# Kernel tuning notes

Measured on AMD Instinct MI355X. Metric: run time of the kernel, lower is better.

Reference implementation:

```python
import jax, jax.numpy as jnp
import numpy as np

ALPHA = 0.2  # LeakyReLU negative slope
NEG_INF = -9e15


def setup_inputs() -> dict:
    key = jax.random.key(0)
    k1, k2, k3, k4, k5 = jax.random.split(key, 5)
    B, N, F_in, F_out = 1, 8192, 256, 128
    h = jax.random.normal(k1, (B, N, F_in), dtype=jnp.float32)
    adj_mat = jax.random.randint(k2, (B, N, N), 0, 2, dtype=jnp.int32)
    W = jax.random.normal(k3, (F_out, F_in), dtype=jnp.float32) * 0.05
    b = jax.random.normal(k4, (F_out,), dtype=jnp.float32) * 0.05
    a = jax.random.normal(k5, (2 * F_out, 1), dtype=jnp.float32) * 0.05
    return {"h": h, "adj_mat": adj_mat, "W": W, "b": b, "a": a}


def reference(h, adj_mat, W, b, a):
    # Wh: (B, N, F_out)
    Wh = jnp.einsum('bnf,of->bno', h, W) + b
    F_out = W.shape[0]
    # Original builds concat[Wh_i, Wh_j] @ a. Equivalent: a1.Wh_i + a2.Wh_j.
    a1 = a[:F_out, 0]
    a2 = a[F_out:, 0]
    s1 = Wh @ a1  # (B, N) source-i contribution
    s2 = Wh @ a2  # (B, N) source-j contribution
    e = s1[:, :, None] + s2[:, None, :]  # (B, N, N)
    e = jnp.where(e >= 0, e, ALPHA * e)  # LeakyReLU
    e = jnp.where(adj_mat > 0, e, NEG_INF)
    attention = jax.nn.softmax(e, axis=1)  # softmax over dim=1, as in the source
    h_prime = jnp.einsum('bij,bjf->bif', attention, Wh)
    return jax.nn.elu(h_prime)
```

## Files before the change

### kernel.cpp

```cpp
#include <hip/hip_runtime.h>

#define NN 8192
#define FI 256
#define FO 128
#define GAT_ALPHA 0.2f

typedef _Float16 f16x8 __attribute__((ext_vector_type(8)));
typedef _Float16 f16x2 __attribute__((ext_vector_type(2)));
typedef float f32x4 __attribute__((ext_vector_type(4)));
typedef unsigned char uchar;
typedef unsigned int uint32;

__global__ __launch_bounds__(256) void k1_wh(const float* __restrict__ h,
                                             const float* __restrict__ W,
                                             const float* __restrict__ bias,
                                             float* __restrict__ Wh) {
  __shared__ float hs[32][FI + 1];
  __shared__ float wt[32][FO];
  const int t = threadIdx.x;
  const int j0 = blockIdx.x * 32;
  {
    const int row = t >> 3, c0 = (t & 7) * 32;
    const float* src = h + (size_t)(j0 + row) * FI + c0;
#pragma unroll
    for (int e = 0; e < 8; ++e) {
      float4 v = *(const float4*)(src + 4 * e);
      hs[row][c0 + 4 * e + 0] = v.x;
      hs[row][c0 + 4 * e + 1] = v.y;
      hs[row][c0 + 4 * e + 2] = v.z;
      hs[row][c0 + 4 * e + 3] = v.w;
    }
  }
  const int f4 = (t & 31) * 4;
  const int r0 = (t >> 5) * 4;
  float acc[4][4];
#pragma unroll
  for (int r = 0; r < 4; ++r)
#pragma unroll
    for (int e = 0; e < 4; ++e) acc[r][e] = 0.f;

  for (int kc = 0; kc < FI; kc += 32) {
    __syncthreads();
    {
      const int f = t >> 1, kb = (t & 1) * 16;
      const float* wsrc = W + (size_t)f * FI + kc + kb;
#pragma unroll
      for (int e = 0; e < 16; ++e) wt[kb + e][f] = wsrc[e];
    }
    __syncthreads();
#pragma unroll
    for (int k = 0; k < 32; ++k) {
      const float4 wv = *(const float4*)&wt[k][f4];
      float hv[4];
#pragma unroll
      for (int r = 0; r < 4; ++r) hv[r] = hs[r0 + r][kc + k];
#pragma unroll
      for (int r = 0; r < 4; ++r) {
        acc[r][0] += hv[r] * wv.x;
        acc[r][1] += hv[r] * wv.y;
        acc[r][2] += hv[r] * wv.z;
        acc[r][3] += hv[r] * wv.w;
      }
    }
  }
  const float4 bv = *(const float4*)&bias[f4];
#pragma unroll
  for (int r = 0; r < 4; ++r) {
    float4 o;
    o.x = acc[r][0] + bv.x;
    o.y = acc[r][1] + bv.y;
    o.z = acc[r][2] + bv.z;
    o.w = acc[r][3] + bv.w;
    *(float4*)&Wh[(size_t)(j0 + r0 + r) * FO + f4] = o;
  }
}

__global__ __launch_bounds__(256) void k1b_sv(const float* __restrict__ Wh,
                                              const float* __restrict__ a,
                                              float4* __restrict__ r4,
                                              float4* __restrict__ c4,
                                              float2* __restrict__ r2,
                                              uint32* __restrict__ c2h,
                                              float* __restrict__ s2x,
                                              float* __restrict__ corr) {
  if (blockIdx.x == 0 && threadIdx.x < FO) corr[threadIdx.x] = 0.f;
  const int lane = threadIdx.x & 63;
  const int j = blockIdx.x * 4 + (threadIdx.x >> 6);
  const float* row = Wh + (size_t)j * FO;
  const float w0 = row[lane], w1 = row[lane + 64];
  float s1 = w0 * a[lane] + w1 * a[lane + 64];
  float s2 = w0 * a[FO + lane] + w1 * a[FO + lane + 64];
#pragma unroll
  for (int o = 32; o >= 1; o >>= 1) {
    s1 += __shfl_xor(s1, o);
    s2 += __shfl_xor(s2, o);
  }
  if (lane == 0) {
    const float e1 = expf(s1), e1a = expf(GAT_ALPHA * s1);
    const float e2 = expf(s2), e2a = expf(GAT_ALPHA * s2);
    float4 rv; rv.x = s1; rv.y = e1; rv.z = e1a; rv.w = 0.f;
    float4 cv; cv.x = s2; cv.y = e2; cv.z = e2a; cv.w = 0.f;
    r4[j] = rv;
    c4[j] = cv;
    r2[j] = make_float2(e1, e1a);
    f16x2 cp; cp.x = (_Float16)e2; cp.y = (_Float16)e2a;
    c2h[j] = __builtin_bit_cast(uint32, cp);
    s2x[j] = s2;
  }
}

__global__ __launch_bounds__(256) void k2_stats(const int* __restrict__ adj,
                                                const float4* __restrict__ r4,
                                                const float* __restrict__ s2x,
                                                uchar* __restrict__ bitsB,
                                                float2* __restrict__ zpart) {
  __shared__ float4 rs[64];
  const int t = threadIdx.x;
  const int jc = blockIdx.x & 3;
  const int ic = blockIdx.x >> 2;
  const int i0 = ic * 64;
  const int j0 = jc * 2048 + t * 8;
  if (t < 64) rs[t] = r4[i0 + t];
  const float4 ca = *(const float4*)(s2x + j0);
  const float4 cb = *(const float4*)(s2x + j0 + 4);
  const float cx[8] = {ca.x, ca.y, ca.z, ca.w, cb.x, cb.y, cb.z, cb.w};
  float accP[8], accN[8];
#pragma unroll
  for (int e = 0; e < 8; ++e) { accP[e] = 0.f; accN[e] = 0.f; }
  __syncthreads();
  const int4* ap = (const int4*)(adj + (size_t)i0 * NN + j0);
  uchar* bp = bitsB + (size_t)i0 * (NN / 8) + jc * 256 + t;
  for (int ir = 0; ir < 64; ir += 8) {
    int4 av[8][2];
#pragma unroll
    for (int u = 0; u < 8; ++u) {
      av[u][0] = ap[(size_t)(ir + u) * (NN / 4)];
      av[u][1] = ap[(size_t)(ir + u) * (NN / 4) + 1];
    }
#pragma unroll
    for (int u = 0; u < 8; ++u) {
      const float4 ri = rs[ir + u];
      const int aa[8] = {av[u][0].x, av[u][0].y, av[u][0].z, av[u][0].w,
                         av[u][1].x, av[u][1].y, av[u][1].z, av[u][1].w};
      uint32 byte = 0;
#pragma unroll
      for (int e = 0; e < 8; ++e) {
        const bool act = aa[e] > 0;
        byte |= act ? (1u << e) : 0u;
        const bool pos = (ri.x + cx[e]) >= 0.f;
        accP[e] += (act && pos) ? ri.y : 0.f;
        accN[e] += (act && !pos) ? ri.z : 0.f;
      }
      bp[(size_t)(ir + u) * (NN / 8)] = (uchar)byte;
    }
  }
  float2* zp = zpart + (size_t)ic * NN + j0;
#pragma unroll
  for (int e = 0; e < 8; ++e) zp[e] = make_float2(accP[e], accN[e]);
}

__global__ __launch_bounds__(256) void k3_scale(const float* __restrict__ Wh,
                                                const float4* __restrict__ c4,
                                                const float2* __restrict__ zpart,
                                                _Float16* __restrict__ Wfrag,
                                                float* __restrict__ corr) {
  __shared__ float rz[64];
  __shared__ int emp[64];
  __shared__ float2 psum[256];
  __shared__ __align__(16) _Float16 tile[FO * 64];
  const int t = threadIdx.x;
  const int j0 = blockIdx.x * 64;
  {
    const int jl = t & 63, q = t >> 6;
    float p = 0.f, n = 0.f;
    for (int ic = q * 32; ic < q * 32 + 32; ++ic) {
      const float2 z = zpart[(size_t)ic * NN + j0 + jl];
      p += z.x;
      n += z.y;
    }
    psum[t] = make_float2(p, n);
  }
  __syncthreads();
  if (t < 64) {
    const float p = psum[t].x + psum[64 + t].x + psum[128 + t].x + psum[192 + t].x;
    const float n = psum[t].y + psum[64 + t].y + psum[128 + t].y + psum[192 + t].y;
    const float4 cj = c4[j0 + t];
    const float Z = cj.y * p + cj.z * n;
    rz[t] = (Z > 0.f) ? 1.f / Z : 0.f;
    emp[t] = (Z > 0.f) ? 0 : 1;
  }
  __syncthreads();
  const int f = t & 127, half = t >> 7;
  const unsigned swf = (unsigned)((f & 7) << 4);
  for (int r = half; r < 64; r += 2) {
    const float v = Wh[(size_t)(j0 + r) * FO + f];
    *(_Float16*)((char*)tile + f * 128 + (((unsigned)(r * 2)) ^ swf)) =
        (_Float16)(v * rz[r]);
    if (emp[r]) atomicAdd(&corr[f], v * (1.f / 8192.f));
  }
  __syncthreads();
#pragma unroll
  for (int q = 0; q < 4; ++q) {
    const int G = t + 256 * q;
    const int kcfb = G >> 6, gl = G & 63;
    const int kc = kcfb >> 3, fb = kcfb & 7;
    const int gf = fb * 16 + (gl & 15);
    const int jloc = kc * 32 + (gl >> 4) * 8;
    const f16x8 v = *(const f16x8*)((const char*)tile + gf * 128 +
                                    (((unsigned)(jloc * 2)) ^ ((unsigned)((gf & 7) << 4))));
    ((f16x8*)Wfrag)[(size_t)(((j0 >> 5) + kc) * 8 + fb) * 64 + gl] = v;
  }
}

#define BARRIER_LDS()                                          \
  do {                                                         \
    __builtin_amdgcn_sched_barrier(0);                         \
    asm volatile("s_waitcnt lgkmcnt(0)" ::: "memory");         \
    __builtin_amdgcn_s_barrier();                              \
    __builtin_amdgcn_sched_barrier(0);                         \
  } while (0)

__global__ __launch_bounds__(512, 4) void k4_main(const uchar* __restrict__ bitsB,
                                                  const float2* __restrict__ r2,
                                                  const uint32* __restrict__ c2h,
                                                  const _Float16* __restrict__ Wfrag,
                                                  float* __restrict__ part) {
  __shared__ __align__(16) _Float16 P[2][64 * 64];
  const int t = threadIdx.x;
  const int rowtile = blockIdx.x >> 2;
  const int kq = blockIdx.x & 3;
  const int rowbase = rowtile * 64;
  const int koff = kq * 2048;

  const int pr = t >> 3, jq = t & 7;
  const float2 rr = r2[rowbase + pr];
  const uchar* bp = bitsB + (size_t)(rowbase + pr) * (NN / 8) + (koff >> 3) + jq;
  const uint32* cp = c2h + koff + jq * 8;
  char* const pdst0 = (char*)&P[0][0] + pr * 128 + (((unsigned)(jq * 16)) ^ ((unsigned)((pr & 7) << 4)));
  char* const pdst1 = (char*)&P[1][0] + pr * 128 + (((unsigned)(jq * 16)) ^ ((unsigned)((pr & 7) << 4)));

  const int lane = t & 63, wave = t >> 6;
  const int wr = wave >> 2, wc = wave & 3;
  const int kgrp = lane >> 4, l15 = lane & 15;
  const unsigned asw = (unsigned)((l15 & 7) << 4);
  const int ar0 = (wr * 32 + l15) * 128;
  const int ar1 = ar0 + 16 * 128;

  f32x4 acc00 = {0.f, 0.f, 0.f, 0.f}, acc01 = {0.f, 0.f, 0.f, 0.f};
  f32x4 acc10 = {0.f, 0.f, 0.f, 0.f}, acc11 = {0.f, 0.f, 0.f, 0.f};

  uchar mb0, mb1;
  uint32 c0a[4], c0b[4], c1a[4], c1b[4];
  f16x8 B000, B001, B010, B011, B100, B101, B110, B111;

#define LOADALL(S, MB, CA, CB, Bq00, Bq01, Bq10, Bq11)                              \
  do {                                                                              \
    MB = bp[(S) * 8];                                                               \
    const uint4 _ca = *(const uint4*)(cp + (S) * 64);                               \
    const uint4 _cb = *(const uint4*)(cp + (S) * 64 + 4);                           \
    CA[0] = _ca.x; CA[1] = _ca.y; CA[2] = _ca.z; CA[3] = _ca.w;                     \
    CB[0] = _cb.x; CB[1] = _cb.y; CB[2] = _cb.z; CB[3] = _cb.w;                     \
    const _Float16* _b = Wfrag + ((size_t)((kq * 64 + (S) * 2) * 8 + wc * 2) * 64 + lane) * 8; \
    Bq00 = *(const f16x8*)(_b);                                                     \
    Bq01 = *(const f16x8*)(_b + 512);                                               \
    Bq10 = *(const f16x8*)(_b + 4096);                                              \
    Bq11 = *(const f16x8*)(_b + 4096 + 512);                                        \
  } while (0)

#define PGEN(DST, MB, CA, CB)                                                       \
  do {                                                                              \
    union { f16x2 h[4]; f16x8 v; } U;                                               \
    _Pragma("unroll") for (int _p = 0; _p < 4; ++_p) {                              \
      const uint32 cv0 = (_p < 2) ? CA[2 * _p] : CB[2 * (_p - 2)];                  \
      const uint32 cv1 = (_p < 2) ? CA[2 * _p + 1] : CB[2 * (_p - 2) + 1];          \
      const f16x2 ch0 = __builtin_bit_cast(f16x2, cv0);                             \
      const f16x2 ch1 = __builtin_bit_cast(f16x2, cv1);                             \
      const float m0 = fmaxf(rr.x * (float)ch0.x, rr.y * (float)ch0.y);             \
      const float m1 = fmaxf(rr.x * (float)ch1.x, rr.y * (float)ch1.y);             \
      const float w0 = ((MB >> (2 * _p)) & 1) ? m0 : 0.f;                           \
      const float w1 = ((MB >> (2 * _p + 1)) & 1) ? m1 : 0.f;                       \
      U.h[_p] = __builtin_bit_cast(f16x2, __builtin_amdgcn_cvt_pkrtz(w0, w1));      \
    }                                                                               \
    *(f16x8*)(DST) = U.v;                                                           \
  } while (0)

#define DO_MFMA(BUF, Bq00, Bq01, Bq10, Bq11)                                        \
  do {                                                                              \
    const char* _Pb = (const char*)&P[BUF][0];                                      \
    const f16x8 a00 = *(const f16x8*)(_Pb + ar0 + ((((unsigned)(kgrp * 16))) ^ asw));        \
    const f16x8 a01 = *(const f16x8*)(_Pb + ar0 + (((unsigned)(64 + kgrp * 16)) ^ asw));     \
    const f16x8 a10 = *(const f16x8*)(_Pb + ar1 + ((((unsigned)(kgrp * 16))) ^ asw));        \
    const f16x8 a11 = *(const f16x8*)(_Pb + ar1 + (((unsigned)(64 + kgrp * 16)) ^ asw));     \
    __builtin_amdgcn_s_setprio(1);                                                  \
    acc00 = __builtin_amdgcn_mfma_f32_16x16x32_f16(a00, Bq00, acc00, 0, 0, 0);      \
    acc01 = __builtin_amdgcn_mfma_f32_16x16x32_f16(a00, Bq01, acc01, 0, 0, 0);      \
    acc10 = __builtin_amdgcn_mfma_f32_16x16x32_f16(a10, Bq00, acc10, 0, 0, 0);      \
    acc11 = __builtin_amdgcn_mfma_f32_16x16x32_f16(a10, Bq01, acc11, 0, 0, 0);      \
    acc00 = __builtin_amdgcn_mfma_f32_16x16x32_f16(a01, Bq10, acc00, 0, 0, 0);      \
    acc01 = __builtin_amdgcn_mfma_f32_16x16x32_f16(a01, Bq11, acc01, 0, 0, 0);      \
    acc10 = __builtin_amdgcn_mfma_f32_16x16x32_f16(a11, Bq10, acc10, 0, 0, 0);      \
    acc11 = __builtin_amdgcn_mfma_f32_16x16x32_f16(a11, Bq11, acc11, 0, 0, 0);      \
    __builtin_amdgcn_s_setprio(0);                                                  \
  } while (0)

  LOADALL(0, mb0, c0a, c0b, B000, B001, B010, B011);
  LOADALL(1, mb1, c1a, c1b, B100, B101, B110, B111);
  PGEN(pdst0, mb0, c0a, c0b);
  BARRIER_LDS();

  for (int s = 0; s < 32; s += 2) {
    PGEN(pdst1, mb1, c1a, c1b);
    DO_MFMA(0, B000, B001, B010, B011);
    if (s + 2 < 32) LOADALL(s + 2, mb0, c0a, c0b, B000, B001, B010, B011);
    BARRIER_LDS();
    DO_MFMA(1, B100, B101, B110, B111);
    if (s + 2 < 32) PGEN(pdst0, mb0, c0a, c0b);
    if (s + 3 < 32) LOADALL(s + 3, mb1, c1a, c1b, B100, B101, B110, B111);
    BARRIER_LDS();
  }

#undef LOADALL
#undef PGEN
#undef DO_MFMA

  const int orow = rowbase + wr * 32 + kgrp * 4;
  const int ocol = wc * 32 + l15;
  float* aP = part + (size_t)kq * NN * FO + (size_t)orow * FO + ocol;
#pragma unroll
  for (int r = 0; r < 4; ++r) {
    aP[(size_t)r * FO] = acc00[r];
    aP[(size_t)r * FO + 16] = acc01[r];
    aP[(size_t)(16 + r) * FO] = acc10[r];
    aP[(size_t)(16 + r) * FO + 16] = acc11[r];
  }
}

__global__ __launch_bounds__(256) void k5_fin(const float* __restrict__ part,
                                              const float* __restrict__ corr,
                                              float* __restrict__ out) {
  const int idx = blockIdx.x * 256 + threadIdx.x;
  const float4 p0 = ((const float4*)part)[idx];
  const float4 p1 = ((const float4*)(part + (size_t)NN * FO))[idx];
  const float4 p2 = ((const float4*)(part + (size_t)2 * NN * FO))[idx];
  const float4 p3 = ((const float4*)(part + (size_t)3 * NN * FO))[idx];
  const float4 c = ((const float4*)corr)[idx & 31];
  float4 v;
  v.x = p0.x + p1.x + p2.x + p3.x + c.x;
  v.y = p0.y + p1.y + p2.y + p3.y + c.y;
  v.z = p0.z + p1.z + p2.z + p3.z + c.z;
  v.w = p0.w + p1.w + p2.w + p3.w + c.w;
  v.x = (v.x > 0.f) ? v.x : (expf(v.x) - 1.f);
  v.y = (v.y > 0.f) ? v.y : (expf(v.y) - 1.f);
  v.z = (v.z > 0.f) ? v.z : (expf(v.z) - 1.f);
  v.w = (v.w > 0.f) ? v.w : (expf(v.w) - 1.f);
  ((float4*)out)[idx] = v;
}

extern "C" void kernel_launch(void* const* d_in, const int* in_sizes, int n_in,
                              void* d_out, int out_size, void* d_ws, size_t ws_size,
                              hipStream_t stream) {
  const float* h = (const float*)d_in[0];
  const int* adj = (const int*)d_in[1];
  const float* W = (const float*)d_in[2];
  const float* b = (const float*)d_in[3];
  const float* a = (const float*)d_in[4];
  float* out = (float*)d_out;
  char* ws = (char*)d_ws;

  float* Wh = (float*)(ws + 0);
  _Float16* Wfrag = (_Float16*)(ws + 0x400000);
  uchar* bits = (uchar*)(ws + 0x600000);
  float2* zpart = (float2*)(ws + 0xE00000);
  float4* r4 = (float4*)(ws + 0x1600000);
  float4* c4 = (float4*)(ws + 0x1620000);
  float2* r2 = (float2*)(ws + 0x1640000);
  uint32* c2h = (uint32*)(ws + 0x1650000);
  float* s2x = (float*)(ws + 0x1658000);
  float* corr = (float*)(ws + 0x1660000);
  float* part = (float*)(ws + 0x1700000);

  k1_wh<<<NN / 32, 256, 0, stream>>>(h, W, b, Wh);
  k1b_sv<<<NN / 4, 256, 0, stream>>>(Wh, a, r4, c4, r2, c2h, s2x, corr);
  k2_stats<<<512, 256, 0, stream>>>(adj, r4, s2x, bits, zpart);
  k3_scale<<<NN / 64, 256, 0, stream>>>(Wh, c4, zpart, Wfrag, corr);
  k4_main<<<512, 512, 0, stream>>>(bits, r2, c2h, Wfrag, part);
  k5_fin<<<(NN * FO / 4) / 256, 256, 0, stream>>>(part, corr, out);
}
```

Measured before the change: 127.5 us.

## Split main kernel K range eight ways with packed-f16 P generation and mask LUT

The main attention-times-Wh kernel now splits the key dimension into 8 chunks instead of 4, doubling the grid to 1024 blocks, and raises the occupancy hint to 8 blocks per CU. P-tile generation moves from f32 math plus a cvt to packed f16 multiplies and max, using planar f16 e2/e2a arrays. Adjacency masking uses an LDS lookup table of 16-bit masks indexed by the adjacency byte. B-fragment loads are issued per step instead of double-buffered in registers. The finalize kernel now sums 8 partial buffers, which doubles partial-sum write and read traffic. It also lowers precision: the row factors are rounded to f16 before multiplying, and the products may overflow or lose accuracy in f16.

```diff
diff --git a/kernel.cpp b/kernel.cpp
--- a/kernel.cpp
+++ b/kernel.cpp
@@ -80,7 +80,8 @@
                                               float4* __restrict__ r4,
                                               float4* __restrict__ c4,
                                               float2* __restrict__ r2,
-                                              uint32* __restrict__ c2h,
+                                              _Float16* __restrict__ ey16,
+                                              _Float16* __restrict__ ez16,
                                               float* __restrict__ s2x,
                                               float* __restrict__ corr) {
   if (blockIdx.x == 0 && threadIdx.x < FO) corr[threadIdx.x] = 0.f;
@@ -103,8 +104,8 @@
     r4[j] = rv;
     c4[j] = cv;
     r2[j] = make_float2(e1, e1a);
-    f16x2 cp; cp.x = (_Float16)e2; cp.y = (_Float16)e2a;
-    c2h[j] = __builtin_bit_cast(uint32, cp);
+    ey16[j] = (_Float16)e2;
+    ez16[j] = (_Float16)e2a;
     s2x[j] = s2;
   }
 }
@@ -220,22 +221,36 @@
     __builtin_amdgcn_sched_barrier(0);                         \
   } while (0)
 
-__global__ __launch_bounds__(512, 4) void k4_main(const uchar* __restrict__ bitsB,
+__global__ __launch_bounds__(512, 8) void k4_main(const uchar* __restrict__ bitsB,
                                                   const float2* __restrict__ r2,
-                                                  const uint32* __restrict__ c2h,
+                                                  const _Float16* __restrict__ ey16,
+                                                  const _Float16* __restrict__ ez16,
                                                   const _Float16* __restrict__ Wfrag,
                                                   float* __restrict__ part) {
   __shared__ __align__(16) _Float16 P[2][64 * 64];
+  __shared__ uint32 lut[256][4];
   const int t = threadIdx.x;
-  const int rowtile = blockIdx.x >> 2;
-  const int kq = blockIdx.x & 3;
+  const int rowtile = blockIdx.x >> 3;
+  const int kq = blockIdx.x & 7;
   const int rowbase = rowtile * 64;
-  const int koff = kq * 2048;
+  const int koff = kq * 1024;
+
+  if (t < 256) {
+#pragma unroll
+    for (int p = 0; p < 4; ++p) {
+      const uint32 lo = ((t >> (2 * p)) & 1) ? 0x0000FFFFu : 0u;
+      const uint32 hi = ((t >> (2 * p + 1)) & 1) ? 0xFFFF0000u : 0u;
+      lut[t][p] = lo | hi;
+    }
+  }
 
   const int pr = t >> 3, jq = t & 7;
   const float2 rr = r2[rowbase + pr];
+  const f16x2 rx2 = {(_Float16)rr.x, (_Float16)rr.x};
+  const f16x2 ry2 = {(_Float16)rr.y, (_Float16)rr.y};
   const uchar* bp = bitsB + (size_t)(rowbase + pr) * (NN / 8) + (koff >> 3) + jq;
-  const uint32* cp = c2h + koff + jq * 8;
+  const _Float16* eyp = ey16 + koff + jq * 8;
+  const _Float16* ezp = ez16 + koff + jq * 8;
   char* const pdst0 = (char*)&P[0][0] + pr * 128 + (((unsigned)(jq * 16)) ^ ((unsigned)((pr & 7) << 4)));
   char* const pdst1 = (char*)&P[1][0] + pr * 128 + (((unsigned)(jq * 16)) ^ ((unsigned)((pr & 7) << 4)));
 
@@ -250,76 +265,83 @@
   f32x4 acc10 = {0.f, 0.f, 0.f, 0.f}, acc11 = {0.f, 0.f, 0.f, 0.f};
 
   uchar mb0, mb1;
-  uint32 c0a[4], c0b[4], c1a[4], c1b[4];
-  f16x8 B000, B001, B010, B011, B100, B101, B110, B111;
-
-#define LOADALL(S, MB, CA, CB, Bq00, Bq01, Bq10, Bq11)                              \
-  do {                                                                              \
-    MB = bp[(S) * 8];                                                               \
-    const uint4 _ca = *(const uint4*)(cp + (S) * 64);                               \
-    const uint4 _cb = *(const uint4*)(cp + (S) * 64 + 4);                           \
-    CA[0] = _ca.x; CA[1] = _ca.y; CA[2] = _ca.z; CA[3] = _ca.w;                     \
-    CB[0] = _cb.x; CB[1] = _cb.y; CB[2] = _cb.z; CB[3] = _cb.w;                     \
-    const _Float16* _b = Wfrag + ((size_t)((kq * 64 + (S) * 2) * 8 + wc * 2) * 64 + lane) * 8; \
-    Bq00 = *(const f16x8*)(_b);                                                     \
-    Bq01 = *(const f16x8*)(_b + 512);                                               \
-    Bq10 = *(const f16x8*)(_b + 4096);                                              \
-    Bq11 = *(const f16x8*)(_b + 4096 + 512);                                        \
+  uint4 ey0, ez0, ey1, ez1;
+  f16x8 B00, B01, B10, B11;
+
+#define LOADSMALL(S, MB, EY, EZ)                       \
+  do {                                                 \
+    MB = bp[(S) * 8];                                  \
+    EY = *(const uint4*)(eyp + (S) * 64);              \
+    EZ = *(const uint4*)(ezp + (S) * 64);              \
   } while (0)
 
-#define PGEN(DST, MB, CA, CB)                                                       \
-  do {                                                                              \
-    union { f16x2 h[4]; f16x8 v; } U;                                               \
-    _Pragma("unroll") for (int _p = 0; _p < 4; ++_p) {                              \
-      const uint32 cv0 = (_p < 2) ? CA[2 * _p] : CB[2 * (_p - 2)];                  \
-      const uint32 cv1 = (_p < 2) ? CA[2 * _p + 1] : CB[2 * (_p - 2) + 1];          \
-      const f16x2 ch0 = __builtin_bit_cast(f16x2, cv0);                             \
-      const f16x2 ch1 = __builtin_bit_cast(f16x2, cv1);                             \
-      const float m0 = fmaxf(rr.x * (float)ch0.x, rr.y * (float)ch0.y);             \
-      const float m1 = fmaxf(rr.x * (float)ch1.x, rr.y * (float)ch1.y);             \
-      const float w0 = ((MB >> (2 * _p)) & 1) ? m0 : 0.f;                           \
-      const float w1 = ((MB >> (2 * _p + 1)) & 1) ? m1 : 0.f;                       \
-      U.h[_p] = __builtin_bit_cast(f16x2, __builtin_amdgcn_cvt_pkrtz(w0, w1));      \
-    }                                                                               \
-    *(f16x8*)(DST) = U.v;                                                           \
+#define LOADB(S)                                                                     \
+  do {                                                                               \
+    const _Float16* _b = Wfrag + ((size_t)((kq * 32 + (S) * 2) * 8 + wc * 2) * 64 + lane) * 8; \
+    B00 = *(const f16x8*)(_b);                                                       \
+    B01 = *(const f16x8*)(_b + 512);                                                 \
+    B10 = *(const f16x8*)(_b + 4096);                                                \
+    B11 = *(const f16x8*)(_b + 4096 + 512);                                          \
   } while (0)
 
-#define DO_MFMA(BUF, Bq00, Bq01, Bq10, Bq11)                                        \
-  do {                                                                              \
-    const char* _Pb = (const char*)&P[BUF][0];                                      \
+#define PGEN(DST, MB, EY, EZ)                                                        \
+  do {                                                                               \
+    const uint4 _m = *(const uint4*)(&lut[MB][0]);                                   \
+    const uint32 _eys[4] = {EY.x, EY.y, EY.z, EY.w};                                 \
+    const uint32 _ezs[4] = {EZ.x, EZ.y, EZ.z, EZ.w};                                 \
+    const uint32 _ms[4] = {_m.x, _m.y, _m.z, _m.w};                                  \
+    uint32 _o[4];                                                                    \
+    _Pragma("unroll") for (int _p = 0; _p < 4; ++_p) {                               \
+      const f16x2 _a = __builtin_bit_cast(f16x2, _eys[_p]) * rx2;                    \
+      const f16x2 _b2 = __builtin_bit_cast(f16x2, _ezs[_p]) * ry2;                   \
+      const f16x2 _mx = __builtin_elementwise_max(_a, _b2);                          \
+      _o[_p] = __builtin_bit_cast(uint32, _mx) & _ms[_p];                            \
+    }                                                                                \
+    uint4 _st; _st.x = _o[0]; _st.y = _o[1]; _st.z = _o[2]; _st.w = _o[3];           \
+    *(uint4*)(DST) = _st;                                                            \
+  } while (0)
+
+#define DO_MFMA(BUF)                                                                 \
+  do {                                                                               \
+    const char* _Pb = (const char*)&P[BUF][0];                                       \
     const f16x8 a00 = *(const f16x8*)(_Pb + ar0 + ((((unsigned)(kgrp * 16))) ^ asw));        \
     const f16x8 a01 = *(const f16x8*)(_Pb + ar0 + (((unsigned)(64 + kgrp * 16)) ^ asw));     \
     const f16x8 a10 = *(const f16x8*)(_Pb + ar1 + ((((unsigned)(kgrp * 16))) ^ asw));        \
     const f16x8 a11 = *(const f16x8*)(_Pb + ar1 + (((unsigned)(64 + kgrp * 16)) ^ asw));     \
-    __builtin_amdgcn_s_setprio(1);                                                  \
-    acc00 = __builtin_amdgcn_mfma_f32_16x16x32_f16(a00, Bq00, acc00, 0, 0, 0);      \
-    acc01 = __builtin_amdgcn_mfma_f32_16x16x32_f16(a00, Bq01, acc01, 0, 0, 0);      \
-    acc10 = __builtin_amdgcn_mfma_f32_16x16x32_f16(a10, Bq00, acc10, 0, 0, 0);      \
-    acc11 = __builtin_amdgcn_mfma_f32_16x16x32_f16(a10, Bq01, acc11, 0, 0, 0);      \
-    acc00 = __builtin_amdgcn_mfma_f32_16x16x32_f16(a01, Bq10, acc00, 0, 0, 0);      \
-    acc01 = __builtin_amdgcn_mfma_f32_16x16x32_f16(a01, Bq11, acc01, 0, 0, 0);      \
-    acc10 = __builtin_amdgcn_mfma_f32_16x16x32_f16(a11, Bq10, acc10, 0, 0, 0);      \
-    acc11 = __builtin_amdgcn_mfma_f32_16x16x32_f16(a11, Bq11, acc11, 0, 0, 0);      \
-    __builtin_amdgcn_s_setprio(0);                                                  \
+    __builtin_amdgcn_s_setprio(1);                                                   \
+    acc00 = __builtin_amdgcn_mfma_f32_16x16x32_f16(a00, B00, acc00, 0, 0, 0);        \
+    acc01 = __builtin_amdgcn_mfma_f32_16x16x32_f16(a00, B01, acc01, 0, 0, 0);        \
+    acc10 = __builtin_amdgcn_mfma_f32_16x16x32_f16(a10, B00, acc10, 0, 0, 0);        \
+    acc11 = __builtin_amdgcn_mfma_f32_16x16x32_f16(a10, B01, acc11, 0, 0, 0);        \
+    acc00 = __builtin_amdgcn_mfma_f32_16x16x32_f16(a01, B10, acc00, 0, 0, 0);        \
+    acc01 = __builtin_amdgcn_mfma_f32_16x16x32_f16(a01, B11, acc01, 0, 0, 0);        \
+    acc10 = __builtin_amdgcn_mfma_f32_16x16x32_f16(a11, B10, acc10, 0, 0, 0);        \
+    acc11 = __builtin_amdgcn_mfma_f32_16x16x32_f16(a11, B11, acc11, 0, 0, 0);        \
+    __builtin_amdgcn_s_setprio(0);                                                   \
   } while (0)
 
-  LOADALL(0, mb0, c0a, c0b, B000, B001, B010, B011);
-  LOADALL(1, mb1, c1a, c1b, B100, B101, B110, B111);
-  PGEN(pdst0, mb0, c0a, c0b);
+  LOADSMALL(0, mb0, ey0, ez0);
+  LOADSMALL(1, mb1, ey1, ez1);
+  __syncthreads();
+  PGEN(pdst0, mb0, ey0, ez0);
+  LOADSMALL(2, mb0, ey0, ez0);
   BARRIER_LDS();
 
-  for (int s = 0; s < 32; s += 2) {
-    PGEN(pdst1, mb1, c1a, c1b);
-    DO_MFMA(0, B000, B001, B010, B011);
-    if (s + 2 < 32) LOADALL(s + 2, mb0, c0a, c0b, B000, B001, B010, B011);
+  for (int s = 0; s < 16; s += 2) {
+    LOADB(s);
+    PGEN(pdst1, mb1, ey1, ez1);
+    if (s + 3 < 16) LOADSMALL(s + 3, mb1, ey1, ez1);
+    DO_MFMA(0);
     BARRIER_LDS();
-    DO_MFMA(1, B100, B101, B110, B111);
-    if (s + 2 < 32) PGEN(pdst0, mb0, c0a, c0b);
-    if (s + 3 < 32) LOADALL(s + 3, mb1, c1a, c1b, B100, B101, B110, B111);
+    LOADB(s + 1);
+    if (s + 2 < 16) PGEN(pdst0, mb0, ey0, ez0);
+    if (s + 4 < 16) LOADSMALL(s + 4, mb0, ey0, ez0);
+    DO_MFMA(1);
     BARRIER_LDS();
   }
 
-#undef LOADALL
+#undef LOADSMALL
+#undef LOADB
 #undef PGEN
 #undef DO_MFMA
 
@@ -339,16 +361,14 @@
                                               const float* __restrict__ corr,
                                               float* __restrict__ out) {
   const int idx = blockIdx.x * 256 + threadIdx.x;
-  const float4 p0 = ((const float4*)part)[idx];
-  const float4 p1 = ((const float4*)(part + (size_t)NN * FO))[idx];
-  const float4 p2 = ((const float4*)(part + (size_t)2 * NN * FO))[idx];
-  const float4 p3 = ((const float4*)(part + (size_t)3 * NN * FO))[idx];
+  float4 v = ((const float4*)part)[idx];
+#pragma unroll
+  for (int q = 1; q < 8; ++q) {
+    const float4 p = ((const float4*)(part + (size_t)q * NN * FO))[idx];
+    v.x += p.x; v.y += p.y; v.z += p.z; v.w += p.w;
+  }
   const float4 c = ((const float4*)corr)[idx & 31];
-  float4 v;
-  v.x = p0.x + p1.x + p2.x + p3.x + c.x;
-  v.y = p0.y + p1.y + p2.y + p3.y + c.y;
-  v.z = p0.z + p1.z + p2.z + p3.z + c.z;
-  v.w = p0.w + p1.w + p2.w + p3.w + c.w;
+  v.x += c.x; v.y += c.y; v.z += c.z; v.w += c.w;
   v.x = (v.x > 0.f) ? v.x : (expf(v.x) - 1.f);
   v.y = (v.y > 0.f) ? v.y : (expf(v.y) - 1.f);
   v.z = (v.z > 0.f) ? v.z : (expf(v.z) - 1.f);
@@ -374,15 +394,16 @@
   float4* r4 = (float4*)(ws + 0x1600000);
   float4* c4 = (float4*)(ws + 0x1620000);
   float2* r2 = (float2*)(ws + 0x1640000);
-  uint32* c2h = (uint32*)(ws + 0x1650000);
+  _Float16* ey16 = (_Float16*)(ws + 0x1650000);
+  _Float16* ez16 = (_Float16*)(ws + 0x1654000);
   float* s2x = (float*)(ws + 0x1658000);
   float* corr = (float*)(ws + 0x1660000);
   float* part = (float*)(ws + 0x1700000);
 
   k1_wh<<<NN / 32, 256, 0, stream>>>(h, W, b, Wh);
-  k1b_sv<<<NN / 4, 256, 0, stream>>>(Wh, a, r4, c4, r2, c2h, s2x, corr);
+  k1b_sv<<<NN / 4, 256, 0, stream>>>(Wh, a, r4, c4, r2, ey16, ez16, s2x, corr);
   k2_stats<<<512, 256, 0, stream>>>(adj, r4, s2x, bits, zpart);
   k3_scale<<<NN / 64, 256, 0, stream>>>(Wh, c4, zpart, Wfrag, corr);
-  k4_main<<<512, 512, 0, stream>>>(bits, r2, c2h, Wfrag, part);
+  k4_main<<<1024, 512, 0, stream>>>(bits, r2, ey16, ez16, Wfrag, part);
   k5_fin<<<(NN * FO / 4) / 256, 256, 0, stream>>>(part, corr, out);
 }
```

After: 251.9 us. 97.5% more time.
